# Optimization experiments

Measured on AMD Instinct MI355X. Metric: run time of the kernel, lower is better.

The kernel has to match this reference:

```python
import jax, jax.numpy as jnp
import numpy as np

TEMP_LEN = 16
TARGET_LEN = 22
DIM = 768
HEADS = 12
B = 16
NT = TEMP_LEN * TEMP_LEN          # 256 template tokens
NG = TARGET_LEN * TARGET_LEN      # 484 target tokens
N = NT + NG                       # 740
POS_HID = 512


def _gaussian_heatmap(center, size, sig=1.0):
    x_axis = np.linspace(0, size[0] - 1, size[0]) - center[0]
    y_axis = np.linspace(0, size[1] - 1, size[1]) - center[1]
    xx, yy = np.meshgrid(x_axis, y_axis)
    return np.exp(-0.5 * (xx ** 2 + yy ** 2) / sig ** 2)


def _bias_index(L):
    # faithful to getBiasIndex (w_len == h_len here)
    coords = np.stack(np.meshgrid(np.arange(L), np.arange(L), indexing='ij'))  # [2,L,L]
    flat = coords.reshape(2, -1)                                               # [2,L*L]
    rel = (flat[:, :, None] - flat[:, None, :]).transpose(1, 2, 0).astype(np.int64)
    rel[:, :, 0] += L - 1
    rel[:, :, 1] += L - 1
    rel[:, :, 0] *= 2 * L - 1
    return rel.sum(-1)  # [L*L, L*L]


def setup_inputs() -> dict:
    key = jax.random.key(0)
    ks = jax.random.split(key, 12)
    f32 = jnp.float32
    x = jax.random.normal(ks[0], (B, N, DIM), dtype=f32)
    temp_q = jax.random.normal(ks[1], (B, NT, DIM), dtype=f32)
    target_q = jax.random.normal(ks[2], (B, NG, DIM), dtype=f32)
    # linear weights stored [in, out] (transposed torch layout)
    w = lambda k, i, o: jax.random.normal(k, (i, o), dtype=f32) * 0.02
    q_w = w(ks[3], DIM, DIM)
    k_w = w(ks[4], DIM, DIM)
    v_w = w(ks[5], DIM, DIM)
    proj_w = w(ks[6], DIM, DIM)
    proj_b = jnp.zeros((DIM,), dtype=f32)
    rpb_table = jax.random.normal(ks[7], ((2 * TARGET_LEN - 1) ** 2, HEADS), dtype=f32) * 0.0002
    rpb_table_temp = jax.random.normal(ks[8], ((2 * TEMP_LEN - 1) ** 2, HEADS), dtype=f32) * 0.0002
    pos_w1 = w(ks[9], 2, POS_HID)
    pos_b1 = jnp.zeros((POS_HID,), dtype=f32)
    pos_w2 = w(ks[10], POS_HID, HEADS)
    pos_b2 = jnp.zeros((HEADS,), dtype=f32)
    # deterministic cross-bias coordinate table (non-learned buffer)
    temp_tab = _gaussian_heatmap((TEMP_LEN // 2, TEMP_LEN // 2), (TEMP_LEN, TEMP_LEN)).astype(np.float32).flatten() \
        + np.linspace(-0.2, 0.2, NT, dtype=np.float32)
    targ_tab = _gaussian_heatmap((TARGET_LEN // 2, TARGET_LEN // 2), (TARGET_LEN, TARGET_LEN)).astype(np.float32).flatten() \
        + np.linspace(-0.2, 0.2, NG, dtype=np.float32)
    # torch.meshgrid default indexing='ij': [2, NT, NG] -> permute(1,2,0) -> [NT,NG,2]
    temp_target = np.stack(np.meshgrid(temp_tab, targ_tab, indexing='ij')).transpose(1, 2, 0)
    target_temp_tab = jnp.asarray(temp_target.transpose(1, 0, 2))  # [NG, NT, 2]
    temp_idx = jnp.asarray(_bias_index(TEMP_LEN))       # [NT, NT] int64
    target_idx = jnp.asarray(_bias_index(TARGET_LEN))   # [NG, NG] int64
    return {
        'x': x, 'temp_q': temp_q, 'target_q': target_q,
        'q_w': q_w, 'k_w': k_w, 'v_w': v_w, 'proj_w': proj_w, 'proj_b': proj_b,
        'rpb_table': rpb_table, 'rpb_table_temp': rpb_table_temp,
        'pos_w1': pos_w1, 'pos_b1': pos_b1, 'pos_w2': pos_w2, 'pos_b2': pos_b2,
        'target_temp_tab': target_temp_tab,
        'temp_idx': temp_idx, 'target_idx': target_idx,
    }


def reference(x, temp_q, target_q, q_w, k_w, v_w, proj_w, proj_b,
              rpb_table, rpb_table_temp, pos_w1, pos_b1, pos_w2, pos_b2,
              target_temp_tab, temp_idx, target_idx):
    Bsz, Ntok, C = x.shape
    H = HEADS
    hd = C // H
    scale = hd ** -0.5

    q_in = jnp.concatenate([temp_q, target_q], axis=1)                 # [B,N,C]
    q = (q_in @ q_w).reshape(Bsz, Ntok, H, hd).transpose(0, 2, 1, 3)   # [B,H,N,hd]
    k = (x @ k_w).reshape(Bsz, Ntok, H, hd).transpose(0, 2, 1, 3)
    v = (x @ v_w).reshape(Bsz, Ntok, H, hd).transpose(0, 2, 1, 3)

    # gathered relative position biases -> [H, Ni, Ni]
    temp_rpb = rpb_table_temp[temp_idx.reshape(-1)].reshape(NT, NT, H).transpose(2, 0, 1)
    targ_rpb = rpb_table[target_idx.reshape(-1)].reshape(NG, NG, H).transpose(2, 0, 1)
    # MLP cross bias: [NG, NT, 2] -> [NG, NT, H] -> [H, NG, NT]
    hid = jax.nn.relu(target_temp_tab @ pos_w1 + pos_b1)
    target_temp_bias = (hid @ pos_w2 + pos_b2).transpose(2, 0, 1)      # [H,NG,NT]
    temp_target_bias = target_temp_bias.transpose(0, 2, 1)             # [H,NT,NG]
    top = jnp.concatenate([temp_rpb, temp_target_bias], axis=2)        # [H,NT,N]
    bot = jnp.concatenate([target_temp_bias, targ_rpb], axis=2)        # [H,NG,N]
    bias = jnp.concatenate([top, bot], axis=1)[None]                   # [1,H,N,N]

    attn = jnp.einsum('bhnd,bhmd->bhnm', q, k) * scale + bias
    attn = jax.nn.softmax(attn, axis=-1)
    out = jnp.einsum('bhnm,bhmd->bhnd', attn, v).transpose(0, 2, 1, 3).reshape(Bsz, Ntok, C)
    return out @ proj_w + proj_b
```

## Files before the change

### kernel.cpp

```cpp
#include <hip/hip_runtime.h>


typedef unsigned short u16;
typedef short bf16x8 __attribute__((ext_vector_type(8)));
typedef float f32x4 __attribute__((ext_vector_type(4)));

#define BSZ   16
#define NTOK  740
#define NTMP  256
#define NTGT  484
#define DIMC  768
#define NHEAD 12
#define HDIM  64
#define MROWS (BSZ*NTOK)
#define LOG2E 1.44269504f
#define NEGS  (-23.0831032f)

__device__ __forceinline__ float bflo(unsigned int u) {
    return __uint_as_float(u << 16);
}
__device__ __forceinline__ float bfhi(unsigned int u) {
    return __uint_as_float(u & 0xffff0000u);
}
__device__ __forceinline__ u16 f2bf(float f) {
    unsigned int u = __float_as_uint(f);
    u += 0x7fffu + ((u >> 16) & 1u);
    return (u16)(u >> 16);
}

__device__ __forceinline__ void gl_lds16(const u16* g, u16* l) {
    __builtin_amdgcn_global_load_lds(
        (const __attribute__((address_space(1))) unsigned int*)(unsigned long long)g,
        (__attribute__((address_space(3))) unsigned int*)(unsigned int)(unsigned long long)l,
        16, 0, 0);
}

__device__ __forceinline__ size_t b2off(int h, int i, int j) {
    return ((size_t)(h * NTOK + i)) * 768 + ((j >> 6) << 6) + ((j & 15) << 2) + ((j >> 4) & 3);
}

#define PREP_MLP  484
#define PREP_CONV (PREP_MLP + 2220)
#define PREP_TRW  (PREP_CONV + 576)
#define PREP_ALL  (PREP_TRW + 2220)

__global__ __launch_bounds__(256) void prep_kernel(
    const float* __restrict__ x, const float* __restrict__ tq,
    const float* __restrict__ gq, u16* __restrict__ XB, u16* __restrict__ QB,
    const float* __restrict__ w0, const float* __restrict__ w1,
    const float* __restrict__ w2, const float* __restrict__ w3,
    u16* __restrict__ Wt,
    const float* __restrict__ rpb, const float* __restrict__ rpbt,
    const int* __restrict__ tidx, const int* __restrict__ gidx,
    const float* __restrict__ pw1, const float* __restrict__ pb1,
    const float* __restrict__ pw2, const float* __restrict__ pb2,
    const float* __restrict__ tab, u16* __restrict__ bias)
{
    __shared__ float T[64][65];
    const int blk = blockIdx.x;
    const int tid = threadIdx.x;

    if (blk < PREP_MLP) {
        int g = blk;
        int t = tid;
        float a  = tab[(g * NTMP + t) * 2 + 0];
        float bb = tab[(g * NTMP + t) * 2 + 1];
        float acc[NHEAD];
        #pragma unroll
        for (int h = 0; h < NHEAD; h++) acc[h] = pb2[h];
        for (int k = 0; k < 512; k++) {
            float hid = fmaxf(a * pw1[k] + bb * pw1[512 + k] + pb1[k], 0.0f);
            #pragma unroll
            for (int h = 0; h < NHEAD; h++) acc[h] += hid * pw2[k * NHEAD + h];
        }
        #pragma unroll
        for (int h = 0; h < NHEAD; h++) {
            u16 v = f2bf(acc[h] * LOG2E);
            bias[b2off(h, t, NTMP + g)] = v;
            bias[b2off(h, NTMP + g, t)] = v;
        }
    } else if (blk < PREP_CONV) {
        int t0 = (blk - PREP_MLP) * 512 + tid;
        int t1 = t0 + 256;
        const float* xs0 = x + (size_t)t0 * 8;
        const float* xs1 = x + (size_t)t1 * 8;
        float4 xa0 = ((const float4*)xs0)[0], xa1 = ((const float4*)xs0)[1];
        float4 xb0 = ((const float4*)xs1)[0], xb1 = ((const float4*)xs1)[1];
        int r0 = t0 / 96, cc0 = (t0 - r0 * 96) * 8;
        int b0 = r0 / NTOK, n0 = r0 - b0 * NTOK;
        const float* qs0 = (n0 < NTMP)
                         ? tq + ((size_t)(b0 * NTMP + n0)) * DIMC + cc0
                         : gq + ((size_t)(b0 * NTGT + (n0 - NTMP))) * DIMC + cc0;
        int r1 = t1 / 96, cc1 = (t1 - r1 * 96) * 8;
        int b1 = r1 / NTOK, n1 = r1 - b1 * NTOK;
        const float* qs1 = (n1 < NTMP)
                         ? tq + ((size_t)(b1 * NTMP + n1)) * DIMC + cc1
                         : gq + ((size_t)(b1 * NTGT + (n1 - NTMP))) * DIMC + cc1;
        float4 qa0 = ((const float4*)qs0)[0], qa1 = ((const float4*)qs0)[1];
        float4 qb0 = ((const float4*)qs1)[0], qb1 = ((const float4*)qs1)[1];
        {
            u16 e[8] = {f2bf(xa0.x), f2bf(xa0.y), f2bf(xa0.z), f2bf(xa0.w),
                        f2bf(xa1.x), f2bf(xa1.y), f2bf(xa1.z), f2bf(xa1.w)};
            *(uint4*)(XB + (size_t)t0 * 8) = *(uint4*)e;
        }
        {
            u16 e[8] = {f2bf(xb0.x), f2bf(xb0.y), f2bf(xb0.z), f2bf(xb0.w),
                        f2bf(xb1.x), f2bf(xb1.y), f2bf(xb1.z), f2bf(xb1.w)};
            *(uint4*)(XB + (size_t)t1 * 8) = *(uint4*)e;
        }
        {
            u16 e[8] = {f2bf(qa0.x), f2bf(qa0.y), f2bf(qa0.z), f2bf(qa0.w),
                        f2bf(qa1.x), f2bf(qa1.y), f2bf(qa1.z), f2bf(qa1.w)};
            *(uint4*)(QB + (size_t)r0 * DIMC + cc0) = *(uint4*)e;
        }
        {
            u16 e[8] = {f2bf(qb0.x), f2bf(qb0.y), f2bf(qb0.z), f2bf(qb0.w),
                        f2bf(qb1.x), f2bf(qb1.y), f2bf(qb1.z), f2bf(qb1.w)};
            *(uint4*)(QB + (size_t)r1 * DIMC + cc1) = *(uint4*)e;
        }
    } else if (blk < PREP_TRW) {
        int t = blk - PREP_CONV;
        int z = t / 144, rem = t - z * 144;
        int bx = rem % 12, by = rem / 12;
        const float* src = (z == 0) ? w0 : (z == 1) ? w1 : (z == 2) ? w2 : w3;
        const float scale = (z == 0) ? 0.125f * LOG2E : 1.0f;
        u16* dst = Wt + (size_t)z * DIMC * DIMC;
        int out0 = bx * 64, in0 = by * 64;
        #pragma unroll
        for (int l = 0; l < 4; l++) {
            int u = tid + (l << 8);
            int r = u >> 4, c4 = (u & 15) << 2;
            float4 p = *(const float4*)(src + (size_t)(in0 + r) * DIMC + out0 + c4);
            T[r][c4] = p.x; T[r][c4 + 1] = p.y; T[r][c4 + 2] = p.z; T[r][c4 + 3] = p.w;
        }
        __syncthreads();
        #pragma unroll
        for (int l = 0; l < 2; l++) {
            int u = tid + (l << 8);
            int r = u >> 3, c8 = (u & 7) << 3;
            u16 e[8];
            #pragma unroll
            for (int i = 0; i < 8; i++) e[i] = f2bf(T[c8 + i][r] * scale);
            *(uint4*)(dst + (size_t)(out0 + r) * DIMC + in0 + c8) = *(uint4*)e;
        }
    } else {
        int t = blk - PREP_TRW;
        int jb = t % 3, i = t / 3;
        int j = jb * 256 + tid;
        u16 vals[NHEAD];
        if (j >= NTOK) {
            u16 neg = f2bf(-1e30f);
            #pragma unroll
            for (int h = 0; h < NHEAD; h++) vals[h] = neg;
        } else if (i < NTMP && j < NTMP) {
            int idx = tidx[i * NTMP + j];
            #pragma unroll
            for (int h = 0; h < NHEAD; h++) vals[h] = f2bf(rpbt[idx * NHEAD + h] * LOG2E);
        } else if (i >= NTMP && j >= NTMP) {
            int idx = gidx[(i - NTMP) * NTGT + (j - NTMP)];
            #pragma unroll
            for (int h = 0; h < NHEAD; h++) vals[h] = f2bf(rpb[idx * NHEAD + h] * LOG2E);
        } else {
            return;
        }
        #pragma unroll
        for (int h = 0; h < NHEAD; h++) vals[h], bias[b2off(h, i, j)] = vals[h];
    }
}

template<int MODE>
__global__ __launch_bounds__(256) void gemm_bf16(
    const u16* __restrict__ A, const u16* __restrict__ Wt,
    const float* __restrict__ pb, u16* __restrict__ C0,
    u16* __restrict__ C1, float* __restrict__ Cf)
{
    __shared__ __align__(16) u16 As[4096];
    __shared__ __align__(16) u16 Bs[8192];
    const int tid = threadIdx.x;
    const int lane = tid & 63, w = tid >> 6;
    const int quad = lane >> 4, ln = lane & 15;

    const int gx = gridDim.x;
    const int nwg = gx * (int)gridDim.y;
    const int flat = blockIdx.y * gx + blockIdx.x;
    const int q = nwg >> 3, r = nwg & 7;
    const int xcd = flat & 7, sidx = flat >> 3;
    const int wg = (xcd < r) ? xcd * (q + 1) + sidx
                             : r * (q + 1) + (xcd - r) * q + sidx;
    const int by = wg / gx, bx = wg - by * gx;

    const int m0 = by << 6;
    const int wm = (w >> 1) << 5, wn = (w & 1) << 6;

    const int nn = bx << 7;
    const u16* Wbase = Wt + (size_t)nn * DIMC;
    u16* Cb;
    int col0;
    if (MODE == 1) {
        if (nn < DIMC) { col0 = nn; Cb = C0; }
        else           { col0 = nn - DIMC; Cb = C1; }
    } else {
        col0 = nn; Cb = C0;
    }

    f32x4 acc[2][4];
    #pragma unroll
    for (int i = 0; i < 2; i++)
        #pragma unroll
        for (int j = 0; j < 4; j++)
            acc[i][j] = (f32x4){0.f, 0.f, 0.f, 0.f};

    #pragma unroll 1
    for (int t = 0; t < 12; t++) {
        __syncthreads();
        const int k0 = t << 6;
        #pragma unroll
        for (int l = 0; l < 2; l++) {
            int f = tid + (l << 8);
            int c8 = f >> 6, rr = f & 63;
            gl_lds16(A + (size_t)(m0 + rr) * DIMC + k0 + c8 * 8, &As[f * 8]);
        }
        #pragma unroll
        for (int l = 0; l < 4; l++) {
            int f = tid + (l << 8);
            int c8 = f >> 7, rr = f & 127;
            gl_lds16(Wbase + (size_t)rr * DIMC + k0 + c8 * 8, &Bs[f * 8]);
        }
        __syncthreads();
        #pragma unroll
        for (int kp = 0; kp < 2; kp++) {
            bf16x8 af[2], bfr[4];
            #pragma unroll
            for (int mt = 0; mt < 2; mt++)
                af[mt] = *(const bf16x8*)
                    &As[(((kp << 2) + quad) * 64 + wm + mt * 16 + ln) * 8];
            #pragma unroll
            for (int nt = 0; nt < 4; nt++)
                bfr[nt] = *(const bf16x8*)
                    &Bs[(((kp << 2) + quad) * 128 + wn + nt * 16 + ln) * 8];
            #pragma unroll
            for (int mt = 0; mt < 2; mt++)
                #pragma unroll
                for (int nt = 0; nt < 4; nt++)
                    acc[mt][nt] = __builtin_amdgcn_mfma_f32_16x16x32_bf16(
                        af[mt], bfr[nt], acc[mt][nt], 0, 0, 0);
        }
    }

    #pragma unroll
    for (int mt = 0; mt < 2; mt++) {
        #pragma unroll
        for (int reg = 0; reg < 4; reg++) {
            int grow = m0 + wm + mt * 16 + (quad << 2) + reg;
            #pragma unroll
            for (int nt = 0; nt < 4; nt++) {
                int gcol = col0 + wn + nt * 16 + ln;
                float v = acc[mt][nt][reg];
                if (MODE == 2) {
                    Cf[(size_t)grow * DIMC + gcol] = v + pb[gcol];
                } else {
                    Cb[(size_t)grow * DIMC + gcol] = f2bf(v);
                }
            }
        }
    }
}

__global__ __launch_bounds__(256) void attn_mfma(
    const u16* __restrict__ Qg, const u16* __restrict__ Kg,
    const u16* __restrict__ Vg, const u16* __restrict__ bias,
    u16* __restrict__ ctx)
{
    __shared__ __align__(16) u16 KsL[4096];
    __shared__ __align__(16) u16 VtL[64 * 72];
    __shared__ __align__(16) u16 Pw[4][16][72];

    const int tid = threadIdx.x;
    const int lane = tid & 63, w = tid >> 6;
    const int quad = lane >> 4, ln = lane & 15;

    const int flat = (blockIdx.z * 12 + blockIdx.y) * 12 + blockIdx.x;
    const int wg = (flat & 7) * 288 + (flat >> 3);
    const int h = wg / 192;
    const int rem = wg - h * 192;
    const int b = rem / 12;
    const int q0 = (rem - b * 12) << 6;

    const int mbase = q0 + (w << 4);
    const u16* bp = bias + ((size_t)h * NTOK) * 768;

    bf16x8 aq[2];
    {
        int qrow = mbase + ln; if (qrow >= NTOK) qrow = NTOK - 1;
        #pragma unroll
        for (int kp = 0; kp < 2; kp++)
            aq[kp] = *(const bf16x8*)(Qg + ((size_t)(b * NTOK + qrow)) * DIMC
                                      + h * HDIM + kp * 32 + (quad << 3));
    }
    int boff[4];
    #pragma unroll
    for (int reg = 0; reg < 4; reg++) {
        int rr = mbase + (quad << 2) + reg;
        if (rr >= NTOK) rr = NTOK - 1;
        boff[reg] = rr * 768 + (ln << 2);
    }

    const int pswz = ((ln >> 2) & 3) << 4;

    float rs[4] = {};
    f32x4 O[4];
    #pragma unroll
    for (int dt = 0; dt < 4; dt++) O[dt] = (f32x4){0.f, 0.f, 0.f, 0.f};

    for (int j0 = 0; j0 < NTOK; j0 += 64) {
        __syncthreads();
        #pragma unroll
        for (int l = 0; l < 2; l++) {
            int f = tid + (l << 8);
            int chunk = f >> 6, jr = f & 63;
            int krow = j0 + jr; if (krow >= NTOK) krow = NTOK - 1;
            gl_lds16(Kg + ((size_t)(b * NTOK + krow)) * DIMC + h * HDIM + chunk * 8,
                     KsL + f * 8);
        }
        uint2 bvv[4];
        #pragma unroll
        for (int reg = 0; reg < 4; reg++)
            bvv[reg] = *(const uint2*)(bp + boff[reg] + j0);
        #pragma unroll
        for (int l = 0; l < 2; l++) {
            int u = tid + (l << 8);
            int jr = u >> 3, d0 = (u & 7) << 3;
            int vrow = j0 + jr; if (vrow >= NTOK) vrow = NTOK - 1;
            uint4 p = *(const uint4*)(Vg + ((size_t)(b * NTOK + vrow)) * DIMC + h * HDIM + d0);
            const u16* pe = (const u16*)&p;
            int jswz = jr ^ d0;
            #pragma unroll
            for (int i = 0; i < 8; i++) VtL[(d0 + i) * 72 + jswz] = pe[i];
        }
        __syncthreads();

        bf16x8 bv[4][2];
        #pragma unroll
        for (int dt = 0; dt < 4; dt++) {
            int key8 = ((dt * 2 + (ln >> 3)) & 7) << 3;
            #pragma unroll
            for (int kp = 0; kp < 2; kp++) {
                int koff = (kp * 32 + (quad << 3)) ^ key8;
                bv[dt][kp] = *(const bf16x8*)&VtL[(dt * 16 + ln) * 72 + koff];
            }
        }

        f32x4 s[4];
        #pragma unroll
        for (int nt = 0; nt < 4; nt++) s[nt] = (f32x4){NEGS, NEGS, NEGS, NEGS};
        __builtin_amdgcn_s_setprio(1);
        #pragma unroll
        for (int kp = 0; kp < 2; kp++)
            #pragma unroll
            for (int nt = 0; nt < 4; nt++) {
                bf16x8 bk = *(const bf16x8*)
                    &KsL[(((kp << 2) + quad) * 64 + nt * 16 + ln) * 8];
                s[nt] = __builtin_amdgcn_mfma_f32_16x16x32_bf16(aq[kp], bk, s[nt], 0, 0, 0);
            }
        __builtin_amdgcn_s_setprio(0);

        #pragma unroll
        for (int reg = 0; reg < 4; reg++) {
            uint2 bb = bvv[reg];
            float p0 = __builtin_exp2f(s[0][reg] + bflo(bb.x));
            float p1 = __builtin_exp2f(s[1][reg] + bfhi(bb.x));
            float p2 = __builtin_exp2f(s[2][reg] + bflo(bb.y));
            float p3 = __builtin_exp2f(s[3][reg] + bfhi(bb.y));
            s[0][reg] = p0; s[1][reg] = p1;
            s[2][reg] = p2; s[3][reg] = p3;
            rs[reg] += p0 + p1 + p2 + p3;
        }
        u16* pwb = &Pw[w][0][0];
        #pragma unroll
        for (int nt = 0; nt < 4; nt++) {
            int colw = ((nt ^ quad) << 4) + ln;
            #pragma unroll
            for (int reg = 0; reg < 4; reg++)
                pwb[((quad << 2) + reg) * 72 + colw] = f2bf(s[nt][reg]);
        }
        bf16x8 ap[2];
        #pragma unroll
        for (int kp = 0; kp < 2; kp++) {
            int koff = (kp * 32 + (quad << 3)) ^ pswz;
            ap[kp] = *(const bf16x8*)&pwb[ln * 72 + koff];
        }
        __builtin_amdgcn_s_setprio(1);
        #pragma unroll
        for (int dt = 0; dt < 4; dt++)
            #pragma unroll
            for (int kp = 0; kp < 2; kp++)
                O[dt] = __builtin_amdgcn_mfma_f32_16x16x32_bf16(
                    ap[kp], bv[dt][kp], O[dt], 0, 0, 0);
        __builtin_amdgcn_s_setprio(0);
    }

    #pragma unroll
    for (int reg = 0; reg < 4; reg++) {
        float t = rs[reg];
        #pragma unroll
        for (int mk = 8; mk >= 1; mk >>= 1) t += __shfl_xor(t, mk);
        float inv = 1.0f / t;
        int row = mbase + (quad << 2) + reg;
        if (row < NTOK) {
            #pragma unroll
            for (int dt = 0; dt < 4; dt++)
                ctx[((size_t)(b * NTOK + row)) * DIMC + h * HDIM + dt * 16 + ln]
                    = f2bf(O[dt][reg] * inv);
        }
    }
}

extern "C" void kernel_launch(void* const* d_in, const int* in_sizes, int n_in,
                              void* d_out, int out_size, void* d_ws, size_t ws_size,
                              hipStream_t stream)
{
    const float* x        = (const float*)d_in[0];
    const float* temp_q   = (const float*)d_in[1];
    const float* target_q = (const float*)d_in[2];
    const float* q_w      = (const float*)d_in[3];
    const float* k_w      = (const float*)d_in[4];
    const float* v_w      = (const float*)d_in[5];
    const float* proj_w   = (const float*)d_in[6];
    const float* proj_b   = (const float*)d_in[7];
    const float* rpb      = (const float*)d_in[8];
    const float* rpbt     = (const float*)d_in[9];
    const float* pw1      = (const float*)d_in[10];
    const float* pb1      = (const float*)d_in[11];
    const float* pw2      = (const float*)d_in[12];
    const float* pb2      = (const float*)d_in[13];
    const float* tab      = (const float*)d_in[14];
    const int*   tidx     = (const int*)d_in[15];
    const int*   gidx     = (const int*)d_in[16];
    float* out = (float*)d_out;

    char* ws = (char*)d_ws;
    const size_t S = (size_t)MROWS * DIMC * sizeof(u16);
    const size_t SZB = (size_t)NHEAD * NTOK * 768 * sizeof(u16);
    u16* XB    = (u16*)(ws);
    u16* QB    = (u16*)(ws + S);
    u16* Q     = (u16*)(ws + 2 * S);
    u16* K     = (u16*)(ws + 3 * S);
    u16* V     = QB;
    u16* CTX   = XB;
    u16* BIAS2 = (u16*)(ws + 4 * S);
    u16* WT    = (u16*)(ws + 4 * S + SZB);

    prep_kernel<<<dim3(PREP_ALL), 256, 0, stream>>>(
        x, temp_q, target_q, XB, QB,
        q_w, k_w, v_w, proj_w, WT,
        rpb, rpbt, tidx, gidx,
        pw1, pb1, pw2, pb2, tab, BIAS2);

    const u16* WTq = WT;
    const u16* WTk = WT + (size_t)DIMC * DIMC;
    const u16* WTp = WT + 3 * (size_t)DIMC * DIMC;

    gemm_bf16<0><<<dim3(6, 185), 256, 0, stream>>>(QB, WTq, nullptr, Q, nullptr, nullptr);
    gemm_bf16<1><<<dim3(12, 185), 256, 0, stream>>>(XB, WTk, nullptr, K, V, nullptr);
    attn_mfma<<<dim3(12, 12, 16), 256, 0, stream>>>(Q, K, V, BIAS2, CTX);
    gemm_bf16<2><<<dim3(6, 185), 256, 0, stream>>>(CTX, WTp, proj_b, nullptr, nullptr, out);
}
```

Before: 456.1 us.

## Fuse fp32-to-bf16 activation conversion into a single combined QKV GEMM

Drops the separate conversion pass that wrote bf16 copies of x and the query inputs. The new QKV kernel reads fp32 activations directly, converts them in registers and stores them to LDS. The Q and K/V GEMMs are merged into one launch, with K and V blocks sharing a single A tile across two weight tiles. This removes one launch plus a round trip of activation writes and reads. The cost is that each K/V block now reads fp32 A with plain vector loads instead of async global-to-LDS copies, and uses more LDS and registers.

Result: slower. 473.2 us (+3.8%).

```diff
diff --git a/kernel.cpp b/kernel.cpp
--- a/kernel.cpp
+++ b/kernel.cpp
@@ -40,13 +40,10 @@
 }
 
 #define PREP_MLP  484
-#define PREP_CONV (PREP_MLP + 2220)
-#define PREP_TRW  (PREP_CONV + 576)
+#define PREP_TRW  (PREP_MLP + 576)
 #define PREP_ALL  (PREP_TRW + 2220)
 
 __global__ __launch_bounds__(256) void prep_kernel(
-    const float* __restrict__ x, const float* __restrict__ tq,
-    const float* __restrict__ gq, u16* __restrict__ XB, u16* __restrict__ QB,
     const float* __restrict__ w0, const float* __restrict__ w1,
     const float* __restrict__ w2, const float* __restrict__ w3,
     u16* __restrict__ Wt,
@@ -79,47 +76,8 @@
             bias[b2off(h, t, NTMP + g)] = v;
             bias[b2off(h, NTMP + g, t)] = v;
         }
-    } else if (blk < PREP_CONV) {
-        int t0 = (blk - PREP_MLP) * 512 + tid;
-        int t1 = t0 + 256;
-        const float* xs0 = x + (size_t)t0 * 8;
-        const float* xs1 = x + (size_t)t1 * 8;
-        float4 xa0 = ((const float4*)xs0)[0], xa1 = ((const float4*)xs0)[1];
-        float4 xb0 = ((const float4*)xs1)[0], xb1 = ((const float4*)xs1)[1];
-        int r0 = t0 / 96, cc0 = (t0 - r0 * 96) * 8;
-        int b0 = r0 / NTOK, n0 = r0 - b0 * NTOK;
-        const float* qs0 = (n0 < NTMP)
-                         ? tq + ((size_t)(b0 * NTMP + n0)) * DIMC + cc0
-                         : gq + ((size_t)(b0 * NTGT + (n0 - NTMP))) * DIMC + cc0;
-        int r1 = t1 / 96, cc1 = (t1 - r1 * 96) * 8;
-        int b1 = r1 / NTOK, n1 = r1 - b1 * NTOK;
-        const float* qs1 = (n1 < NTMP)
-                         ? tq + ((size_t)(b1 * NTMP + n1)) * DIMC + cc1
-                         : gq + ((size_t)(b1 * NTGT + (n1 - NTMP))) * DIMC + cc1;
-        float4 qa0 = ((const float4*)qs0)[0], qa1 = ((const float4*)qs0)[1];
-        float4 qb0 = ((const float4*)qs1)[0], qb1 = ((const float4*)qs1)[1];
-        {
-            u16 e[8] = {f2bf(xa0.x), f2bf(xa0.y), f2bf(xa0.z), f2bf(xa0.w),
-                        f2bf(xa1.x), f2bf(xa1.y), f2bf(xa1.z), f2bf(xa1.w)};
-            *(uint4*)(XB + (size_t)t0 * 8) = *(uint4*)e;
-        }
-        {
-            u16 e[8] = {f2bf(xb0.x), f2bf(xb0.y), f2bf(xb0.z), f2bf(xb0.w),
-                        f2bf(xb1.x), f2bf(xb1.y), f2bf(xb1.z), f2bf(xb1.w)};
-            *(uint4*)(XB + (size_t)t1 * 8) = *(uint4*)e;
-        }
-        {
-            u16 e[8] = {f2bf(qa0.x), f2bf(qa0.y), f2bf(qa0.z), f2bf(qa0.w),
-                        f2bf(qa1.x), f2bf(qa1.y), f2bf(qa1.z), f2bf(qa1.w)};
-            *(uint4*)(QB + (size_t)r0 * DIMC + cc0) = *(uint4*)e;
-        }
-        {
-            u16 e[8] = {f2bf(qb0.x), f2bf(qb0.y), f2bf(qb0.z), f2bf(qb0.w),
-                        f2bf(qb1.x), f2bf(qb1.y), f2bf(qb1.z), f2bf(qb1.w)};
-            *(uint4*)(QB + (size_t)r1 * DIMC + cc1) = *(uint4*)e;
-        }
     } else if (blk < PREP_TRW) {
-        int t = blk - PREP_CONV;
+        int t = blk - PREP_MLP;
         int z = t / 144, rem = t - z * 144;
         int bx = rem % 12, by = rem / 12;
         const float* src = (z == 0) ? w0 : (z == 1) ? w1 : (z == 2) ? w2 : w3;
@@ -164,15 +122,178 @@
             return;
         }
         #pragma unroll
-        for (int h = 0; h < NHEAD; h++) vals[h], bias[b2off(h, i, j)] = vals[h];
-    }
-}
-
-template<int MODE>
-__global__ __launch_bounds__(256) void gemm_bf16(
+        for (int h = 0; h < NHEAD; h++) bias[b2off(h, i, j)] = vals[h];
+    }
+}
+
+__global__ __launch_bounds__(256) void gemm_qkv(
+    const float* __restrict__ x, const float* __restrict__ tq,
+    const float* __restrict__ gq, const u16* __restrict__ Wt,
+    u16* __restrict__ Qo, u16* __restrict__ Ko, u16* __restrict__ Vo)
+{
+    __shared__ __align__(16) u16 As[4096];
+    __shared__ __align__(16) u16 Bs0[8192];
+    __shared__ __align__(16) u16 Bs1[8192];
+    const int tid = threadIdx.x;
+    const int lane = tid & 63, w = tid >> 6;
+    const int quad = lane >> 4, ln = lane & 15;
+
+    const int nwg = 12 * 185;
+    const int flat = blockIdx.y * 12 + blockIdx.x;
+    const int q = nwg >> 3, r = nwg & 7;
+    const int xcd = flat & 7, sidx = flat >> 3;
+    const int wg = (xcd < r) ? xcd * (q + 1) + sidx
+                             : r * (q + 1) + (xcd - r) * q + sidx;
+    const int by = wg / 12, bx = wg - by * 12;
+
+    const int m0 = by << 6;
+    const int wm = (w >> 1) << 5, wn = (w & 1) << 6;
+
+    const int rr = tid >> 2, qq = tid & 3;
+    const int arow = m0 + rr;
+
+    if (bx < 6) {
+        const int nn = bx << 7;
+        const u16* Wb = Wt + (size_t)nn * DIMC;
+        int b = arow / NTOK, n = arow - b * NTOK;
+        const float* aptr = (n < NTMP)
+                          ? tq + ((size_t)(b * NTMP + n)) * DIMC
+                          : gq + ((size_t)(b * NTGT + (n - NTMP))) * DIMC;
+
+        f32x4 acc[2][4];
+        #pragma unroll
+        for (int i = 0; i < 2; i++)
+            #pragma unroll
+            for (int j = 0; j < 4; j++) acc[i][j] = (f32x4){0.f, 0.f, 0.f, 0.f};
+
+        #pragma unroll 1
+        for (int t = 0; t < 12; t++) {
+            const int k0 = t << 6;
+            __syncthreads();
+            const float* s = aptr + k0 + (qq << 4);
+            float4 a0 = ((const float4*)s)[0], a1 = ((const float4*)s)[1];
+            float4 a2 = ((const float4*)s)[2], a3 = ((const float4*)s)[3];
+            #pragma unroll
+            for (int l = 0; l < 4; l++) {
+                int f = tid + (l << 8);
+                int c8 = f >> 7, r2 = f & 127;
+                gl_lds16(Wb + (size_t)r2 * DIMC + k0 + c8 * 8, &Bs0[f * 8]);
+            }
+            u16 e[16] = {f2bf(a0.x), f2bf(a0.y), f2bf(a0.z), f2bf(a0.w),
+                         f2bf(a1.x), f2bf(a1.y), f2bf(a1.z), f2bf(a1.w),
+                         f2bf(a2.x), f2bf(a2.y), f2bf(a2.z), f2bf(a2.w),
+                         f2bf(a3.x), f2bf(a3.y), f2bf(a3.z), f2bf(a3.w)};
+            *(uint4*)&As[(((qq << 1) + 0) * 64 + rr) * 8] = ((uint4*)e)[0];
+            *(uint4*)&As[(((qq << 1) + 1) * 64 + rr) * 8] = ((uint4*)e)[1];
+            __syncthreads();
+            #pragma unroll
+            for (int kp = 0; kp < 2; kp++) {
+                bf16x8 af[2], bfr[4];
+                #pragma unroll
+                for (int mt = 0; mt < 2; mt++)
+                    af[mt] = *(const bf16x8*)
+                        &As[(((kp << 2) + quad) * 64 + wm + mt * 16 + ln) * 8];
+                #pragma unroll
+                for (int nt = 0; nt < 4; nt++)
+                    bfr[nt] = *(const bf16x8*)
+                        &Bs0[(((kp << 2) + quad) * 128 + wn + nt * 16 + ln) * 8];
+                #pragma unroll
+                for (int mt = 0; mt < 2; mt++)
+                    #pragma unroll
+                    for (int nt = 0; nt < 4; nt++)
+                        acc[mt][nt] = __builtin_amdgcn_mfma_f32_16x16x32_bf16(
+                            af[mt], bfr[nt], acc[mt][nt], 0, 0, 0);
+            }
+        }
+        #pragma unroll
+        for (int mt = 0; mt < 2; mt++)
+            #pragma unroll
+            for (int reg = 0; reg < 4; reg++) {
+                int grow = m0 + wm + mt * 16 + (quad << 2) + reg;
+                #pragma unroll
+                for (int nt = 0; nt < 4; nt++)
+                    Qo[(size_t)grow * DIMC + nn + wn + nt * 16 + ln]
+                        = f2bf(acc[mt][nt][reg]);
+            }
+    } else {
+        const int nn = (bx - 6) << 7;
+        const u16* Wbk = Wt + (size_t)DIMC * DIMC + (size_t)nn * DIMC;
+        const u16* Wbv = Wt + 2 * (size_t)DIMC * DIMC + (size_t)nn * DIMC;
+        const float* aptr = x + (size_t)arow * DIMC;
+
+        f32x4 ak[2][4], av[2][4];
+        #pragma unroll
+        for (int i = 0; i < 2; i++)
+            #pragma unroll
+            for (int j = 0; j < 4; j++) {
+                ak[i][j] = (f32x4){0.f, 0.f, 0.f, 0.f};
+                av[i][j] = (f32x4){0.f, 0.f, 0.f, 0.f};
+            }
+
+        #pragma unroll 1
+        for (int t = 0; t < 12; t++) {
+            const int k0 = t << 6;
+            __syncthreads();
+            const float* s = aptr + k0 + (qq << 4);
+            float4 a0 = ((const float4*)s)[0], a1 = ((const float4*)s)[1];
+            float4 a2 = ((const float4*)s)[2], a3 = ((const float4*)s)[3];
+            #pragma unroll
+            for (int l = 0; l < 4; l++) {
+                int f = tid + (l << 8);
+                int c8 = f >> 7, r2 = f & 127;
+                gl_lds16(Wbk + (size_t)r2 * DIMC + k0 + c8 * 8, &Bs0[f * 8]);
+                gl_lds16(Wbv + (size_t)r2 * DIMC + k0 + c8 * 8, &Bs1[f * 8]);
+            }
+            u16 e[16] = {f2bf(a0.x), f2bf(a0.y), f2bf(a0.z), f2bf(a0.w),
+                         f2bf(a1.x), f2bf(a1.y), f2bf(a1.z), f2bf(a1.w),
+                         f2bf(a2.x), f2bf(a2.y), f2bf(a2.z), f2bf(a2.w),
+                         f2bf(a3.x), f2bf(a3.y), f2bf(a3.z), f2bf(a3.w)};
+            *(uint4*)&As[(((qq << 1) + 0) * 64 + rr) * 8] = ((uint4*)e)[0];
+            *(uint4*)&As[(((qq << 1) + 1) * 64 + rr) * 8] = ((uint4*)e)[1];
+            __syncthreads();
+            #pragma unroll
+            for (int kp = 0; kp < 2; kp++) {
+                bf16x8 af[2], bk[4], bv[4];
+                #pragma unroll
+                for (int mt = 0; mt < 2; mt++)
+                    af[mt] = *(const bf16x8*)
+                        &As[(((kp << 2) + quad) * 64 + wm + mt * 16 + ln) * 8];
+                #pragma unroll
+                for (int nt = 0; nt < 4; nt++) {
+                    bk[nt] = *(const bf16x8*)
+                        &Bs0[(((kp << 2) + quad) * 128 + wn + nt * 16 + ln) * 8];
+                    bv[nt] = *(const bf16x8*)
+                        &Bs1[(((kp << 2) + quad) * 128 + wn + nt * 16 + ln) * 8];
+                }
+                #pragma unroll
+                for (int mt = 0; mt < 2; mt++)
+                    #pragma unroll
+                    for (int nt = 0; nt < 4; nt++) {
+                        ak[mt][nt] = __builtin_amdgcn_mfma_f32_16x16x32_bf16(
+                            af[mt], bk[nt], ak[mt][nt], 0, 0, 0);
+                        av[mt][nt] = __builtin_amdgcn_mfma_f32_16x16x32_bf16(
+                            af[mt], bv[nt], av[mt][nt], 0, 0, 0);
+                    }
+            }
+        }
+        #pragma unroll
+        for (int mt = 0; mt < 2; mt++)
+            #pragma unroll
+            for (int reg = 0; reg < 4; reg++) {
+                int grow = m0 + wm + mt * 16 + (quad << 2) + reg;
+                #pragma unroll
+                for (int nt = 0; nt < 4; nt++) {
+                    int gcol = nn + wn + nt * 16 + ln;
+                    Ko[(size_t)grow * DIMC + gcol] = f2bf(ak[mt][nt][reg]);
+                    Vo[(size_t)grow * DIMC + gcol] = f2bf(av[mt][nt][reg]);
+                }
+            }
+    }
+}
+
+__global__ __launch_bounds__(256) void gemm_proj(
     const u16* __restrict__ A, const u16* __restrict__ Wt,
-    const float* __restrict__ pb, u16* __restrict__ C0,
-    u16* __restrict__ C1, float* __restrict__ Cf)
+    const float* __restrict__ pb, float* __restrict__ Cf)
 {
     __shared__ __align__(16) u16 As[4096];
     __shared__ __align__(16) u16 Bs[8192];
@@ -180,35 +301,24 @@
     const int lane = tid & 63, w = tid >> 6;
     const int quad = lane >> 4, ln = lane & 15;
 
-    const int gx = gridDim.x;
-    const int nwg = gx * (int)gridDim.y;
-    const int flat = blockIdx.y * gx + blockIdx.x;
+    const int nwg = 6 * 185;
+    const int flat = blockIdx.y * 6 + blockIdx.x;
     const int q = nwg >> 3, r = nwg & 7;
     const int xcd = flat & 7, sidx = flat >> 3;
     const int wg = (xcd < r) ? xcd * (q + 1) + sidx
                              : r * (q + 1) + (xcd - r) * q + sidx;
-    const int by = wg / gx, bx = wg - by * gx;
+    const int by = wg / 6, bx = wg - by * 6;
 
     const int m0 = by << 6;
     const int wm = (w >> 1) << 5, wn = (w & 1) << 6;
-
     const int nn = bx << 7;
-    const u16* Wbase = Wt + (size_t)nn * DIMC;
-    u16* Cb;
-    int col0;
-    if (MODE == 1) {
-        if (nn < DIMC) { col0 = nn; Cb = C0; }
-        else           { col0 = nn - DIMC; Cb = C1; }
-    } else {
-        col0 = nn; Cb = C0;
-    }
+    const u16* Wb = Wt + (size_t)nn * DIMC;
 
     f32x4 acc[2][4];
     #pragma unroll
     for (int i = 0; i < 2; i++)
         #pragma unroll
-        for (int j = 0; j < 4; j++)
-            acc[i][j] = (f32x4){0.f, 0.f, 0.f, 0.f};
+        for (int j = 0; j < 4; j++) acc[i][j] = (f32x4){0.f, 0.f, 0.f, 0.f};
 
     #pragma unroll 1
     for (int t = 0; t < 12; t++) {
@@ -217,14 +327,14 @@
         #pragma unroll
         for (int l = 0; l < 2; l++) {
             int f = tid + (l << 8);
-            int c8 = f >> 6, rr = f & 63;
-            gl_lds16(A + (size_t)(m0 + rr) * DIMC + k0 + c8 * 8, &As[f * 8]);
+            int c8 = f >> 6, r2 = f & 63;
+            gl_lds16(A + (size_t)(m0 + r2) * DIMC + k0 + c8 * 8, &As[f * 8]);
         }
         #pragma unroll
         for (int l = 0; l < 4; l++) {
             int f = tid + (l << 8);
-            int c8 = f >> 7, rr = f & 127;
-            gl_lds16(Wbase + (size_t)rr * DIMC + k0 + c8 * 8, &Bs[f * 8]);
+            int c8 = f >> 7, r2 = f & 127;
+            gl_lds16(Wb + (size_t)r2 * DIMC + k0 + c8 * 8, &Bs[f * 8]);
         }
         __syncthreads();
         #pragma unroll
@@ -248,22 +358,16 @@
     }
 
     #pragma unroll
-    for (int mt = 0; mt < 2; mt++) {
+    for (int mt = 0; mt < 2; mt++)
         #pragma unroll
         for (int reg = 0; reg < 4; reg++) {
             int grow = m0 + wm + mt * 16 + (quad << 2) + reg;
             #pragma unroll
             for (int nt = 0; nt < 4; nt++) {
-                int gcol = col0 + wn + nt * 16 + ln;
-                float v = acc[mt][nt][reg];
-                if (MODE == 2) {
-                    Cf[(size_t)grow * DIMC + gcol] = v + pb[gcol];
-                } else {
-                    Cb[(size_t)grow * DIMC + gcol] = f2bf(v);
-                }
-            }
-        }
-    }
+                int gcol = nn + wn + nt * 16 + ln;
+                Cf[(size_t)grow * DIMC + gcol] = acc[mt][nt][reg] + pb[gcol];
+            }
+        }
 }
 
 __global__ __launch_bounds__(256) void attn_mfma(
@@ -441,27 +545,21 @@
     char* ws = (char*)d_ws;
     const size_t S = (size_t)MROWS * DIMC * sizeof(u16);
     const size_t SZB = (size_t)NHEAD * NTOK * 768 * sizeof(u16);
-    u16* XB    = (u16*)(ws);
-    u16* QB    = (u16*)(ws + S);
+    u16* CTX   = (u16*)(ws);
+    u16* V     = (u16*)(ws + S);
     u16* Q     = (u16*)(ws + 2 * S);
     u16* K     = (u16*)(ws + 3 * S);
-    u16* V     = QB;
-    u16* CTX   = XB;
     u16* BIAS2 = (u16*)(ws + 4 * S);
     u16* WT    = (u16*)(ws + 4 * S + SZB);
 
     prep_kernel<<<dim3(PREP_ALL), 256, 0, stream>>>(
-        x, temp_q, target_q, XB, QB,
         q_w, k_w, v_w, proj_w, WT,
         rpb, rpbt, tidx, gidx,
         pw1, pb1, pw2, pb2, tab, BIAS2);
 
-    const u16* WTq = WT;
-    const u16* WTk = WT + (size_t)DIMC * DIMC;
     const u16* WTp = WT + 3 * (size_t)DIMC * DIMC;
 
-    gemm_bf16<0><<<dim3(6, 185), 256, 0, stream>>>(QB, WTq, nullptr, Q, nullptr, nullptr);
-    gemm_bf16<1><<<dim3(12, 185), 256, 0, stream>>>(XB, WTk, nullptr, K, V, nullptr);
+    gemm_qkv<<<dim3(12, 185), 256, 0, stream>>>(x, temp_q, target_q, WT, Q, K, V);
     attn_mfma<<<dim3(12, 12, 16), 256, 0, stream>>>(Q, K, V, BIAS2, CTX);
-    gemm_bf16<2><<<dim3(6, 185), 256, 0, stream>>>(CTX, WTp, proj_b, nullptr, nullptr, out);
-}
+    gemm_proj<<<dim3(6, 185), 256, 0, stream>>>(CTX, WTp, proj_b, out);
+}
```
